# Performance work log

Measured on AMD Instinct MI355X. Metric: run time of the kernel, lower is better.

The kernel has to match this reference:

```python
import jax, jax.numpy as jnp
import numpy as np


def setup_inputs() -> dict:
    key = jax.random.key(0)
    ks = jax.random.split(key, 4)
    B, C, H, W = 8, 512, 128, 128
    K, D = 150, 512
    std = 0.02
    return {
        "x": jax.random.normal(ks[0], (B, C, H, W), dtype=jnp.float32),
        "cls_repr": jax.random.normal(ks[1], (1, K, D), dtype=jnp.float32) * std,
        "W_cls": jax.random.normal(ks[2], (D, D), dtype=jnp.float32) * std,
        "W_feat": jax.random.normal(ks[3], (D, D), dtype=jnp.float32) * std,
        "ln_gamma": jnp.ones((K,), dtype=jnp.float32),
        "ln_beta": jnp.zeros((K,), dtype=jnp.float32),
    }


def reference(x, cls_repr, W_cls, W_feat, ln_gamma, ln_beta):
    b, c, h, w = x.shape
    K = cls_repr.shape[1]
    # img_feat: [b, hw, c]
    img_feat = jnp.transpose(x, (0, 2, 3, 1)).reshape(b, h * w, c)
    cls = jnp.broadcast_to(cls_repr, (b, K, c))
    # coupled_attn: [b, K, hw]
    coupled_attn = jnp.einsum("bnc,bkc->bkn", img_feat, cls)
    # class-direction softmax over hw, feeds class offsets
    cls_attn = jax.nn.softmax(coupled_attn, axis=2)                 # [b,K,hw]
    cls_offset = jnp.einsum("bkn,bnc->bkc", cls_attn, img_feat) @ W_cls.T
    aligned_cls = cls + cls_offset                                   # [b,K,c]
    # position-direction softmax over K, feeds feature offsets
    pos_attn = jax.nn.softmax(coupled_attn, axis=1)                 # [b,K,hw]
    feat_offset = jnp.einsum("bkn,bkc->bnc", pos_attn, cls) @ W_feat.T
    aligned_feat = img_feat + feat_offset                            # [b,hw,c]
    # masks: [b, hw, K], LayerNorm over K
    masks = jnp.einsum("bnc,bkc->bnk", aligned_feat, aligned_cls)
    mu = jnp.mean(masks, axis=-1, keepdims=True)
    var = jnp.var(masks, axis=-1, keepdims=True)
    masks = (masks - mu) * jax.lax.rsqrt(var + 1e-5) * ln_gamma + ln_beta
    return jnp.transpose(masks, (0, 2, 1)).reshape(b, K, h, w)
```

## Files before the change

### kernel.cpp

```cpp
#include <hip/hip_runtime.h>
#include <math.h>

#define BB 8
#define CC 512
#define HWN 16384
#define KK 150
#define KP 160
#define NSEG 32
#define SEGN (HWN / NSEG)

typedef short bf8v __attribute__((ext_vector_type(8)));
typedef float f4v __attribute__((ext_vector_type(4)));

static __device__ inline unsigned short f2b(float f) {
  unsigned u = __float_as_uint(f);
  u += 0x7fffu + ((u >> 16) & 1u);
  return (unsigned short)(u >> 16);
}
static __device__ inline float b2f(unsigned short s) {
  return __uint_as_float(((unsigned)s) << 16);
}
static __device__ inline float b2fs(short s) { return b2f((unsigned short)s); }

__global__ __launch_bounds__(256) void t0_prep(const float* __restrict__ cls,
                                               unsigned short* __restrict__ cls16,
                                               unsigned short* __restrict__ MT16,
                                               unsigned short* __restrict__ AC16) {
  int i = blockIdx.x * 256 + threadIdx.x;
  if (i < KP * CC) {
    int k = i >> 9, c = i & 511;
    cls16[i] = (k < KK) ? f2b(cls[k * CC + c]) : 0;
  }
  if (i < BB * KP * KP) MT16[i] = 0;
  if (i < BB * (KP - KK) * CC) {
    int b = i / ((KP - KK) * CC);
    int r = i % ((KP - KK) * CC);
    int k = KK + (r >> 9);
    int c = r & 511;
    AC16[((size_t)b * KP + k) * CC + c] = 0;
  }
}

__global__ __launch_bounds__(256) void t1_transpose(const float* __restrict__ x,
                                                    unsigned short* __restrict__ xT) {
  __shared__ float ts[32][65];
  const int n0 = blockIdx.x * 64, c0 = blockIdx.y * 32, b = blockIdx.z;
  const int tid = threadIdx.x;
  const float* xb = x + (size_t)b * CC * HWN;
#pragma unroll
  for (int i = 0; i < 8; i++) {
    int e = tid + i * 256;
    int n = e & 63, c = e >> 6;
    ts[c][n] = xb[(size_t)(c0 + c) * HWN + n0 + n];
  }
  __syncthreads();
  unsigned short* xo = xT + (size_t)b * HWN * CC;
#pragma unroll
  for (int i = 0; i < 4; i++) {
    int e = tid + i * 256;
    int c2 = e & 15, n = e >> 4;
    unsigned vv = (unsigned)f2b(ts[2 * c2][n]) | ((unsigned)f2b(ts[2 * c2 + 1][n]) << 16);
    *(unsigned*)&xo[(size_t)(n0 + n) * CC + c0 + 2 * c2] = vv;
  }
}

__global__ __launch_bounds__(256) void g1_mfma(const unsigned short* __restrict__ xT,
                                               const unsigned short* __restrict__ cls16,
                                               unsigned short* __restrict__ A16,
                                               float* __restrict__ vvec) {
  const int n0 = blockIdx.x * 128, b = blockIdx.y;
  const int tid = threadIdx.x, w = tid >> 6, L = tid & 63;
  const int q = L >> 4, m16 = L & 15;
  f4v zf = {0.f, 0.f, 0.f, 0.f};
  f4v acc[10][2];
#pragma unroll
  for (int mt = 0; mt < 10; mt++) { acc[mt][0] = zf; acc[mt][1] = zf; }
  const unsigned short* xr0 = xT + ((size_t)(b * HWN + n0 + 32 * w + m16)) * CC + 8 * q;
  const unsigned short* xr1 = xr0 + 16 * CC;
  const unsigned short* cb = cls16 + (size_t)m16 * CC + 8 * q;
#pragma unroll 2
  for (int c0 = 0; c0 < CC; c0 += 32) {
    bf8v b0 = *(const bf8v*)(xr0 + c0);
    bf8v b1 = *(const bf8v*)(xr1 + c0);
#pragma unroll
    for (int mt = 0; mt < 10; mt++) {
      bf8v a = *(const bf8v*)(cb + (size_t)(16 * mt) * CC + c0);
      acc[mt][0] = __builtin_amdgcn_mfma_f32_16x16x32_bf16(a, b0, acc[mt][0], 0, 0, 0);
      acc[mt][1] = __builtin_amdgcn_mfma_f32_16x16x32_bf16(a, b1, acc[mt][1], 0, 0, 0);
    }
  }
#pragma unroll
  for (int mt = 0; mt < 10; mt++)
#pragma unroll
    for (int r = 0; r < 4; r++) {
      int k = 16 * mt + 4 * q + r;
      if (k < KK) {
        size_t row = ((size_t)(b * KK + k)) * HWN + n0 + 32 * w;
        A16[row + m16] = f2b(acc[mt][0][r]);
        A16[row + 16 + m16] = f2b(acc[mt][1][r]);
      }
    }
  float cm[2] = {-1e30f, -1e30f}, cs[2] = {0.f, 0.f};
  const int kq = 4 * q;
#pragma unroll
  for (int mt = 0; mt < 10; mt++)
#pragma unroll
    for (int r = 0; r < 4; r++) {
      bool valid = (16 * mt + kq + r) < KK;
#pragma unroll
      for (int nc = 0; nc < 2; nc++) {
        float a = valid ? acc[mt][nc][r] : -1e30f;
        cm[nc] = fmaxf(cm[nc], a);
      }
    }
#pragma unroll
  for (int mt = 0; mt < 10; mt++)
#pragma unroll
    for (int r = 0; r < 4; r++) {
      bool valid = (16 * mt + kq + r) < KK;
#pragma unroll
      for (int nc = 0; nc < 2; nc++)
        if (valid) cs[nc] += __expf(acc[mt][nc][r] - cm[nc]);
    }
#pragma unroll
  for (int off = 16; off < 64; off <<= 1) {
#pragma unroll
    for (int nc = 0; nc < 2; nc++) {
      float m2 = __shfl_xor(cm[nc], off, 64);
      float s2 = __shfl_xor(cs[nc], off, 64);
      float mn = fmaxf(cm[nc], m2);
      cs[nc] = cs[nc] * __expf(cm[nc] - mn) + s2 * __expf(m2 - mn);
      cm[nc] = mn;
    }
  }
  if (q == 0) {
#pragma unroll
    for (int nc = 0; nc < 2; nc++)
      vvec[b * HWN + n0 + 32 * w + 16 * nc + m16] = __expf(-cm[nc]) / cs[nc];
  }
}

__global__ __launch_bounds__(256) void g2a_rowstats(const unsigned short* __restrict__ A16,
                                                    float* __restrict__ rowmax,
                                                    float* __restrict__ rowsum) {
  const int bk = blockIdx.x;
  const bf8v* row = (const bf8v*)(A16 + (size_t)bk * HWN);
  __shared__ float red[8];
  const int tid = threadIdx.x, lane = tid & 63, w = tid >> 6;
  float m = -1e30f;
  for (int i = tid; i < HWN / 8; i += 256) {
    bf8v u = row[i];
#pragma unroll
    for (int j = 0; j < 8; j++) m = fmaxf(m, b2fs(u[j]));
  }
#pragma unroll
  for (int o = 32; o > 0; o >>= 1) m = fmaxf(m, __shfl_down(m, o, 64));
  if (lane == 0) red[w] = m;
  __syncthreads();
  if (tid == 0) red[4] = fmaxf(fmaxf(red[0], red[1]), fmaxf(red[2], red[3]));
  __syncthreads();
  const float mm = red[4];
  float s = 0.f;
  for (int i = tid; i < HWN / 8; i += 256) {
    bf8v u = row[i];
#pragma unroll
    for (int j = 0; j < 8; j++) s += __expf(b2fs(u[j]) - mm);
  }
#pragma unroll
  for (int o = 32; o > 0; o >>= 1) s += __shfl_down(s, o, 64);
  if (lane == 0) red[w] = s;
  __syncthreads();
  if (tid == 0) {
    rowmax[bk] = mm;
    rowsum[bk] = red[0] + red[1] + red[2] + red[3];
  }
}

__global__ __launch_bounds__(256) void e1_exp(const unsigned short* __restrict__ A16,
                                              const float* __restrict__ rowmax,
                                              unsigned short* __restrict__ E16,
                                              unsigned short* __restrict__ ET16) {
  const int n0 = blockIdx.x * 64, k0 = blockIdx.y * 32, b = blockIdx.z;
  const int tid = threadIdx.x;
  __shared__ unsigned short ls[64 * 33];
  const int kr = tid >> 3, n8 = tid & 7;
  const int k = k0 + kr;
  bf8v e;
  if (k < KK) {
    float rm = rowmax[b * KK + k];
    bf8v a = *(const bf8v*)&A16[((size_t)(b * KK + k)) * HWN + n0 + 8 * n8];
#pragma unroll
    for (int j = 0; j < 8; j++) e[j] = (short)f2b(__expf(b2fs(a[j]) - rm));
  } else {
#pragma unroll
    for (int j = 0; j < 8; j++) e[j] = 0;
  }
  *(bf8v*)&E16[((size_t)(b * KP + k)) * HWN + n0 + 8 * n8] = e;
#pragma unroll
  for (int j = 0; j < 8; j++) ls[(8 * n8 + j) * 33 + kr] = (unsigned short)e[j];
  __syncthreads();
  const int n = tid >> 2, k8 = tid & 3;
  bf8v o;
#pragma unroll
  for (int j = 0; j < 8; j++) o[j] = (short)ls[n * 33 + 8 * k8 + j];
  *(bf8v*)&ET16[((size_t)(b * HWN + n0 + n)) * KP + k0 + 8 * k8] = o;
}

__global__ __launch_bounds__(256) void g3_mfma(const float* __restrict__ x,
                                               const unsigned short* __restrict__ E16,
                                               float* __restrict__ Scp) {
  const int cblk = blockIdx.x, seg = blockIdx.y, b = blockIdx.z;
  const int tid = threadIdx.x, w = tid >> 6, L = tid & 63;
  const int q = L >> 4, m16 = L & 15;
  const int kgrp = w & 1, cgrp = w >> 1;
  f4v zf = {0.f, 0.f, 0.f, 0.f};
  f4v acc[5][4];
#pragma unroll
  for (int mt = 0; mt < 5; mt++)
#pragma unroll
    for (int cc = 0; cc < 4; cc++) acc[mt][cc] = zf;
  const unsigned short* eb = E16 + ((size_t)(b * KP + 80 * kgrp + m16)) * HWN + 8 * q;
  const float* xb = x + (size_t)b * CC * HWN +
                    (size_t)(cblk * 128 + 64 * cgrp + m16) * HWN + 8 * q;
  const int ns0 = seg * SEGN;
#pragma unroll 2
  for (int nc0 = ns0; nc0 < ns0 + SEGN; nc0 += 32) {
    bf8v af[5];
#pragma unroll
    for (int mt = 0; mt < 5; mt++)
      af[mt] = *(const bf8v*)(eb + (size_t)(16 * mt) * HWN + nc0);
#pragma unroll
    for (int cc = 0; cc < 4; cc++) {
      const float* xp = xb + (size_t)(16 * cc) * HWN + nc0;
      float4 x0 = *(const float4*)xp;
      float4 x1 = *(const float4*)(xp + 4);
      bf8v bf;
      bf[0] = (short)f2b(x0.x); bf[1] = (short)f2b(x0.y);
      bf[2] = (short)f2b(x0.z); bf[3] = (short)f2b(x0.w);
      bf[4] = (short)f2b(x1.x); bf[5] = (short)f2b(x1.y);
      bf[6] = (short)f2b(x1.z); bf[7] = (short)f2b(x1.w);
#pragma unroll
      for (int mt = 0; mt < 5; mt++)
        acc[mt][cc] = __builtin_amdgcn_mfma_f32_16x16x32_bf16(af[mt], bf, acc[mt][cc], 0, 0, 0);
    }
  }
#pragma unroll
  for (int mt = 0; mt < 5; mt++)
#pragma unroll
    for (int cc = 0; cc < 4; cc++)
#pragma unroll
      for (int r = 0; r < 4; r++) {
        int k = 80 * kgrp + 16 * mt + 4 * q + r;
        if (k < KK) {
          int c = cblk * 128 + 64 * cgrp + 16 * cc + m16;
          Scp[(((size_t)(b * NSEG + seg)) * KK + k) * CC + c] = acc[mt][cc][r];
        }
      }
}

__global__ __launch_bounds__(256) void g5_reduce(const float* __restrict__ Scp,
                                                 const float* __restrict__ rowsum,
                                                 float* __restrict__ Sc) {
  const int bk = blockIdx.x;
  const int b = bk / KK, k = bk % KK;
  const float inv = 1.0f / rowsum[bk];
  for (int c = threadIdx.x; c < CC; c += 256) {
    float s = 0.f;
    for (int g = 0; g < NSEG; g++)
      s += Scp[(((size_t)(b * NSEG + g)) * KK + k) * CC + c];
    Sc[(size_t)bk * CC + c] = s * inv;
  }
}

__global__ __launch_bounds__(256) void g4b_cwf(const float* __restrict__ cls,
                                               const float* __restrict__ Wf,
                                               float* __restrict__ CWf) {
  const int k = blockIdx.y;
  const int w = threadIdx.x >> 6, lane = threadIdx.x & 63;
  const int j0 = (blockIdx.x * 4 + w) * 4;
  const float4* arow = (const float4*)(cls + (size_t)k * CC);
  float4 a0 = arow[lane], a1 = arow[64 + lane];
#pragma unroll
  for (int jj = 0; jj < 4; jj++) {
    const float4* brow = (const float4*)(Wf + (size_t)(j0 + jj) * CC);
    float4 b0 = brow[lane], b1 = brow[64 + lane];
    float d = a0.x * b0.x + a0.y * b0.y + a0.z * b0.z + a0.w * b0.w +
              a1.x * b1.x + a1.y * b1.y + a1.z * b1.z + a1.w * b1.w;
#pragma unroll
    for (int o = 32; o > 0; o >>= 1) d += __shfl_down(d, o, 64);
    if (lane == 0) CWf[(size_t)k * CC + j0 + jj] = d;
  }
}

__global__ __launch_bounds__(256) void g4a_ac(const float* __restrict__ Sc,
                                              const float* __restrict__ Wc,
                                              const float* __restrict__ cls,
                                              float* __restrict__ AC,
                                              unsigned short* __restrict__ AC16) {
  const int bk = blockIdx.y;
  const int b = bk / KK, k = bk % KK;
  const int w = threadIdx.x >> 6, lane = threadIdx.x & 63;
  const int j0 = (blockIdx.x * 4 + w) * 4;
  const float4* arow = (const float4*)(Sc + (size_t)bk * CC);
  float4 a0 = arow[lane], a1 = arow[64 + lane];
#pragma unroll
  for (int jj = 0; jj < 4; jj++) {
    const float4* brow = (const float4*)(Wc + (size_t)(j0 + jj) * CC);
    float4 b0 = brow[lane], b1 = brow[64 + lane];
    float d = a0.x * b0.x + a0.y * b0.y + a0.z * b0.z + a0.w * b0.w +
              a1.x * b1.x + a1.y * b1.y + a1.z * b1.z + a1.w * b1.w;
#pragma unroll
    for (int o = 32; o > 0; o >>= 1) d += __shfl_down(d, o, 64);
    if (lane == 0) {
      float val = cls[k * CC + j0 + jj] + d;
      AC[(size_t)bk * CC + j0 + jj] = val;
      AC16[((size_t)b * KP + k) * CC + j0 + jj] = f2b(val);
    }
  }
}

__global__ __launch_bounds__(256) void g4c_m(const float* __restrict__ CWf,
                                             const float* __restrict__ AC,
                                             const float* __restrict__ rowmax,
                                             unsigned short* __restrict__ MT16) {
  const int k1 = blockIdx.y, b = blockIdx.z;
  const int w = threadIdx.x >> 6, lane = threadIdx.x & 63;
  const int k20 = (blockIdx.x * 4 + w) * 4;
  const float4* arow = (const float4*)(CWf + (size_t)k1 * CC);
  float4 a0 = arow[lane], a1 = arow[64 + lane];
  const float u = __expf(rowmax[b * KK + k1]);
#pragma unroll
  for (int jj = 0; jj < 4; jj++) {
    int k2 = k20 + jj;
    if (k2 >= KK) break;
    const float4* brow = (const float4*)(AC + (size_t)(b * KK + k2) * CC);
    float4 b0 = brow[lane], b1 = brow[64 + lane];
    float d = a0.x * b0.x + a0.y * b0.y + a0.z * b0.z + a0.w * b0.w +
              a1.x * b1.x + a1.y * b1.y + a1.z * b1.z + a1.w * b1.w;
#pragma unroll
    for (int o = 32; o > 0; o >>= 1) d += __shfl_down(d, o, 64);
    if (lane == 0) MT16[((size_t)b * KP + k2) * KP + k1] = f2b(d * u);
  }
}

__global__ __launch_bounds__(256) void g6_mfma(
    const unsigned short* __restrict__ xT, const unsigned short* __restrict__ ET,
    const float* __restrict__ vvec, const unsigned short* __restrict__ AC16,
    const unsigned short* __restrict__ MT16, const float* __restrict__ gamma,
    const float* __restrict__ beta, float* __restrict__ out) {
  const int n0 = blockIdx.x * 128, b = blockIdx.y;
  const int tid = threadIdx.x, w = tid >> 6, L = tid & 63;
  const int q = L >> 4, m16 = L & 15;
  f4v zf = {0.f, 0.f, 0.f, 0.f};
  f4v acc[10][2];
#pragma unroll
  for (int mt = 0; mt < 10; mt++) { acc[mt][0] = zf; acc[mt][1] = zf; }

  const unsigned short* et0 = ET + ((size_t)(b * HWN + n0 + 32 * w + m16)) * KP + 8 * q;
  const unsigned short* et1 = et0 + 16 * KP;
  const unsigned short* mb = MT16 + (size_t)b * KP * KP + (size_t)m16 * KP + 8 * q;
#pragma unroll
  for (int kc = 0; kc < KP; kc += 32) {
    bf8v b0 = *(const bf8v*)(et0 + kc);
    bf8v b1 = *(const bf8v*)(et1 + kc);
#pragma unroll
    for (int mt = 0; mt < 10; mt++) {
      bf8v a = *(const bf8v*)(mb + (size_t)(16 * mt) * KP + kc);
      acc[mt][0] = __builtin_amdgcn_mfma_f32_16x16x32_bf16(a, b0, acc[mt][0], 0, 0, 0);
      acc[mt][1] = __builtin_amdgcn_mfma_f32_16x16x32_bf16(a, b1, acc[mt][1], 0, 0, 0);
    }
  }
  const float v0 = vvec[b * HWN + n0 + 32 * w + m16];
  const float v1 = vvec[b * HWN + n0 + 32 * w + 16 + m16];
#pragma unroll
  for (int mt = 0; mt < 10; mt++)
#pragma unroll
    for (int r = 0; r < 4; r++) {
      acc[mt][0][r] *= v0;
      acc[mt][1][r] *= v1;
    }

  const unsigned short* xr0 = xT + ((size_t)(b * HWN + n0 + 32 * w + m16)) * CC + 8 * q;
  const unsigned short* xr1 = xr0 + 16 * CC;
  const unsigned short* ab = AC16 + (size_t)b * KP * CC + (size_t)m16 * CC + 8 * q;
#pragma unroll 2
  for (int c0 = 0; c0 < CC; c0 += 32) {
    bf8v b0 = *(const bf8v*)(xr0 + c0);
    bf8v b1 = *(const bf8v*)(xr1 + c0);
#pragma unroll
    for (int mt = 0; mt < 10; mt++) {
      bf8v a = *(const bf8v*)(ab + (size_t)(16 * mt) * CC + c0);
      acc[mt][0] = __builtin_amdgcn_mfma_f32_16x16x32_bf16(a, b0, acc[mt][0], 0, 0, 0);
      acc[mt][1] = __builtin_amdgcn_mfma_f32_16x16x32_bf16(a, b1, acc[mt][1], 0, 0, 0);
    }
  }

  float s1[2] = {0.f, 0.f}, s2[2] = {0.f, 0.f};
#pragma unroll
  for (int mt = 0; mt < 10; mt++)
#pragma unroll
    for (int r = 0; r < 4; r++)
#pragma unroll
      for (int nc = 0; nc < 2; nc++) {
        float a = acc[mt][nc][r];
        s1[nc] += a;
        s2[nc] += a * a;
      }
#pragma unroll
  for (int nc = 0; nc < 2; nc++) {
    s1[nc] += __shfl_xor(s1[nc], 16, 64);
    s1[nc] += __shfl_xor(s1[nc], 32, 64);
    s2[nc] += __shfl_xor(s2[nc], 16, 64);
    s2[nc] += __shfl_xor(s2[nc], 32, 64);
  }
  float mu[2], inv[2];
#pragma unroll
  for (int nc = 0; nc < 2; nc++) {
    mu[nc] = s1[nc] * (1.0f / KK);
    float var = s2[nc] * (1.0f / KK) - mu[nc] * mu[nc];
    inv[nc] = rsqrtf(var + 1e-5f);
  }
#pragma unroll
  for (int mt = 0; mt < 10; mt++)
#pragma unroll
    for (int r = 0; r < 4; r++) {
      int k = 16 * mt + 4 * q + r;
      if (k < KK) {
        float g = gamma[k], be = beta[k];
        size_t row = (size_t)(b * KK + k) * HWN + n0 + 32 * w;
        out[row + m16] = (acc[mt][0][r] - mu[0]) * inv[0] * g + be;
        out[row + 16 + m16] = (acc[mt][1][r] - mu[1]) * inv[1] * g + be;
      }
    }
}

extern "C" void kernel_launch(void* const* d_in, const int* in_sizes, int n_in,
                              void* d_out, int out_size, void* d_ws, size_t ws_size,
                              hipStream_t stream) {
  const float* x = (const float*)d_in[0];
  const float* cls = (const float*)d_in[1];
  const float* Wc = (const float*)d_in[2];
  const float* Wf = (const float*)d_in[3];
  const float* gam = (const float*)d_in[4];
  const float* bet = (const float*)d_in[5];
  float* out = (float*)d_out;

  char* p = (char*)d_ws;
  auto alloc = [&](size_t bytes) {
    char* r = p;
    p += (bytes + 255) & ~(size_t)255;
    return r;
  };
  unsigned short* xT16 = (unsigned short*)alloc((size_t)BB * HWN * CC * 2);
  unsigned short* A16 = (unsigned short*)alloc((size_t)BB * KK * HWN * 2);
  unsigned short* E16 = (unsigned short*)alloc((size_t)BB * KP * HWN * 2);
  unsigned short* ET16 = (unsigned short*)alloc((size_t)BB * HWN * KP * 2);
  float* Scp = (float*)alloc((size_t)BB * NSEG * KK * CC * 4);
  float* Sc = (float*)alloc((size_t)BB * KK * CC * 4);
  float* AC = (float*)alloc((size_t)BB * KK * CC * 4);
  unsigned short* AC16 = (unsigned short*)alloc((size_t)BB * KP * CC * 2);
  float* CWf = (float*)alloc((size_t)KK * CC * 4);
  unsigned short* cls16 = (unsigned short*)alloc((size_t)KP * CC * 2);
  unsigned short* MT16 = (unsigned short*)alloc((size_t)BB * KP * KP * 2);
  float* rowmax = (float*)alloc(BB * KK * 4);
  float* rowsum = (float*)alloc(BB * KK * 4);
  float* vvec = (float*)alloc((size_t)BB * HWN * 4);

  t0_prep<<<dim3((BB * KP * KP + 255) / 256), 256, 0, stream>>>(cls, cls16, MT16, AC16);
  t1_transpose<<<dim3(HWN / 64, CC / 32, BB), 256, 0, stream>>>(x, xT16);
  g1_mfma<<<dim3(HWN / 128, BB), 256, 0, stream>>>(xT16, cls16, A16, vvec);
  g2a_rowstats<<<dim3(BB * KK), 256, 0, stream>>>(A16, rowmax, rowsum);
  e1_exp<<<dim3(HWN / 64, KP / 32, BB), 256, 0, stream>>>(A16, rowmax, E16, ET16);
  g3_mfma<<<dim3(CC / 128, NSEG, BB), 256, 0, stream>>>(x, E16, Scp);
  g5_reduce<<<dim3(BB * KK), 256, 0, stream>>>(Scp, rowsum, Sc);
  g4b_cwf<<<dim3(CC / 16, KK), 256, 0, stream>>>(cls, Wf, CWf);
  g4a_ac<<<dim3(CC / 16, BB * KK), 256, 0, stream>>>(Sc, Wc, cls, AC, AC16);
  g4c_m<<<dim3(10, KK, BB), 256, 0, stream>>>(CWf, AC, rowmax, MT16);
  g6_mfma<<<dim3(HWN / 128, BB), 256, 0, stream>>>(xT16, ET16, vvec, AC16, MT16,
                                                   gam, bet, out);
}
```

Before: 930.8 us.

## Fuse softmax exp into first GEMM and move small matmuls to MFMA

The first GEMM now exponentiates its logits directly, with no max subtraction. It writes E16 and ET16, atomically accumulates row sums and computes the column inverse sums, so the A16 buffer and the rowstats and exp kernels are removed. The transpose kernel also writes a bf16 copy of x in the original layout, so g3 reads half the bytes and skips per-iteration conversion. The small class/weight projections (CWf, AC, MT) become bf16 MFMA GEMMs instead of per-dot-product wave reductions. Dropping the max subtraction risks overflow or precision loss if logits are large, and atomics add nondeterminism.

```diff
diff --git a/kernel.cpp b/kernel.cpp
--- a/kernel.cpp
+++ b/kernel.cpp
@@ -23,9 +23,14 @@
 static __device__ inline float b2fs(short s) { return b2f((unsigned short)s); }
 
 __global__ __launch_bounds__(256) void t0_prep(const float* __restrict__ cls,
+                                               const float* __restrict__ Wc,
+                                               const float* __restrict__ Wf,
                                                unsigned short* __restrict__ cls16,
+                                               unsigned short* __restrict__ Wc16,
+                                               unsigned short* __restrict__ Wf16,
                                                unsigned short* __restrict__ MT16,
-                                               unsigned short* __restrict__ AC16) {
+                                               unsigned short* __restrict__ AC16,
+                                               float* __restrict__ rowsum) {
   int i = blockIdx.x * 256 + threadIdx.x;
   if (i < KP * CC) {
     int k = i >> 9, c = i & 511;
@@ -39,19 +44,28 @@
     int c = r & 511;
     AC16[((size_t)b * KP + k) * CC + c] = 0;
   }
+  if (i < CC * CC) {
+    Wc16[i] = f2b(Wc[i]);
+    Wf16[i] = f2b(Wf[i]);
+  }
+  if (i < BB * KK) rowsum[i] = 0.f;
 }
 
 __global__ __launch_bounds__(256) void t1_transpose(const float* __restrict__ x,
-                                                    unsigned short* __restrict__ xT) {
+                                                    unsigned short* __restrict__ xT,
+                                                    unsigned short* __restrict__ x16) {
   __shared__ float ts[32][65];
   const int n0 = blockIdx.x * 64, c0 = blockIdx.y * 32, b = blockIdx.z;
   const int tid = threadIdx.x;
   const float* xb = x + (size_t)b * CC * HWN;
+  unsigned short* x16o = x16 + (size_t)b * CC * HWN;
 #pragma unroll
   for (int i = 0; i < 8; i++) {
     int e = tid + i * 256;
     int n = e & 63, c = e >> 6;
-    ts[c][n] = xb[(size_t)(c0 + c) * HWN + n0 + n];
+    float v = xb[(size_t)(c0 + c) * HWN + n0 + n];
+    ts[c][n] = v;
+    x16o[(size_t)(c0 + c) * HWN + n0 + n] = f2b(v);
   }
   __syncthreads();
   unsigned short* xo = xT + (size_t)b * HWN * CC;
@@ -66,8 +80,10 @@
 
 __global__ __launch_bounds__(256) void g1_mfma(const unsigned short* __restrict__ xT,
                                                const unsigned short* __restrict__ cls16,
-                                               unsigned short* __restrict__ A16,
-                                               float* __restrict__ vvec) {
+                                               unsigned short* __restrict__ E16,
+                                               unsigned short* __restrict__ ET16,
+                                               float* __restrict__ vvec,
+                                               float* __restrict__ rowsum) {
   const int n0 = blockIdx.x * 128, b = blockIdx.y;
   const int tid = threadIdx.x, w = tid >> 6, L = tid & 63;
   const int q = L >> 4, m16 = L & 15;
@@ -89,170 +105,84 @@
       acc[mt][1] = __builtin_amdgcn_mfma_f32_16x16x32_bf16(a, b1, acc[mt][1], 0, 0, 0);
     }
   }
-#pragma unroll
-  for (int mt = 0; mt < 10; mt++)
+  float cs0 = 0.f, cs1 = 0.f;
+  const int nA = n0 + 32 * w + m16;
+#pragma unroll
+  for (int mt = 0; mt < 10; mt++) {
+    unsigned short u0a[4], u1a[4];
 #pragma unroll
     for (int r = 0; r < 4; r++) {
       int k = 16 * mt + 4 * q + r;
-      if (k < KK) {
-        size_t row = ((size_t)(b * KK + k)) * HWN + n0 + 32 * w;
-        A16[row + m16] = f2b(acc[mt][0][r]);
-        A16[row + 16 + m16] = f2b(acc[mt][1][r]);
-      }
-    }
-  float cm[2] = {-1e30f, -1e30f}, cs[2] = {0.f, 0.f};
-  const int kq = 4 * q;
-#pragma unroll
-  for (int mt = 0; mt < 10; mt++)
-#pragma unroll
-    for (int r = 0; r < 4; r++) {
-      bool valid = (16 * mt + kq + r) < KK;
-#pragma unroll
-      for (int nc = 0; nc < 2; nc++) {
-        float a = valid ? acc[mt][nc][r] : -1e30f;
-        cm[nc] = fmaxf(cm[nc], a);
-      }
-    }
-#pragma unroll
-  for (int mt = 0; mt < 10; mt++)
-#pragma unroll
-    for (int r = 0; r < 4; r++) {
-      bool valid = (16 * mt + kq + r) < KK;
-#pragma unroll
-      for (int nc = 0; nc < 2; nc++)
-        if (valid) cs[nc] += __expf(acc[mt][nc][r] - cm[nc]);
-    }
-#pragma unroll
-  for (int off = 16; off < 64; off <<= 1) {
-#pragma unroll
-    for (int nc = 0; nc < 2; nc++) {
-      float m2 = __shfl_xor(cm[nc], off, 64);
-      float s2 = __shfl_xor(cs[nc], off, 64);
-      float mn = fmaxf(cm[nc], m2);
-      cs[nc] = cs[nc] * __expf(cm[nc] - mn) + s2 * __expf(m2 - mn);
-      cm[nc] = mn;
-    }
-  }
+      bool valid = k < KK;
+      float e0 = valid ? __expf(acc[mt][0][r]) : 0.f;
+      float e1 = valid ? __expf(acc[mt][1][r]) : 0.f;
+      cs0 += e0;
+      cs1 += e1;
+      unsigned short u0 = valid ? f2b(e0) : (unsigned short)0;
+      unsigned short u1 = valid ? f2b(e1) : (unsigned short)0;
+      u0a[r] = u0;
+      u1a[r] = u1;
+      size_t row = ((size_t)(b * KP + k)) * HWN + n0 + 32 * w;
+      E16[row + m16] = u0;
+      E16[row + 16 + m16] = u1;
+      float es = e0 + e1;
+      es += __shfl_xor(es, 1, 64);
+      es += __shfl_xor(es, 2, 64);
+      es += __shfl_xor(es, 4, 64);
+      es += __shfl_xor(es, 8, 64);
+      if (valid && m16 == 0) atomicAdd(&rowsum[b * KK + k], es);
+    }
+    unsigned lo0 = (unsigned)u0a[0] | ((unsigned)u0a[1] << 16);
+    unsigned hi0 = (unsigned)u0a[2] | ((unsigned)u0a[3] << 16);
+    unsigned lo1 = (unsigned)u1a[0] | ((unsigned)u1a[1] << 16);
+    unsigned hi1 = (unsigned)u1a[2] | ((unsigned)u1a[3] << 16);
+    size_t eoff = ((size_t)(b * HWN + nA)) * KP + 16 * mt + 4 * q;
+    *(uint2*)&ET16[eoff] = make_uint2(lo0, hi0);
+    *(uint2*)&ET16[eoff + (size_t)16 * KP] = make_uint2(lo1, hi1);
+  }
+  cs0 += __shfl_xor(cs0, 16, 64);
+  cs0 += __shfl_xor(cs0, 32, 64);
+  cs1 += __shfl_xor(cs1, 16, 64);
+  cs1 += __shfl_xor(cs1, 32, 64);
   if (q == 0) {
-#pragma unroll
-    for (int nc = 0; nc < 2; nc++)
-      vvec[b * HWN + n0 + 32 * w + 16 * nc + m16] = __expf(-cm[nc]) / cs[nc];
-  }
-}
-
-__global__ __launch_bounds__(256) void g2a_rowstats(const unsigned short* __restrict__ A16,
-                                                    float* __restrict__ rowmax,
-                                                    float* __restrict__ rowsum) {
-  const int bk = blockIdx.x;
-  const bf8v* row = (const bf8v*)(A16 + (size_t)bk * HWN);
-  __shared__ float red[8];
-  const int tid = threadIdx.x, lane = tid & 63, w = tid >> 6;
-  float m = -1e30f;
-  for (int i = tid; i < HWN / 8; i += 256) {
-    bf8v u = row[i];
-#pragma unroll
-    for (int j = 0; j < 8; j++) m = fmaxf(m, b2fs(u[j]));
-  }
-#pragma unroll
-  for (int o = 32; o > 0; o >>= 1) m = fmaxf(m, __shfl_down(m, o, 64));
-  if (lane == 0) red[w] = m;
-  __syncthreads();
-  if (tid == 0) red[4] = fmaxf(fmaxf(red[0], red[1]), fmaxf(red[2], red[3]));
-  __syncthreads();
-  const float mm = red[4];
-  float s = 0.f;
-  for (int i = tid; i < HWN / 8; i += 256) {
-    bf8v u = row[i];
-#pragma unroll
-    for (int j = 0; j < 8; j++) s += __expf(b2fs(u[j]) - mm);
-  }
-#pragma unroll
-  for (int o = 32; o > 0; o >>= 1) s += __shfl_down(s, o, 64);
-  if (lane == 0) red[w] = s;
-  __syncthreads();
-  if (tid == 0) {
-    rowmax[bk] = mm;
-    rowsum[bk] = red[0] + red[1] + red[2] + red[3];
-  }
-}
-
-__global__ __launch_bounds__(256) void e1_exp(const unsigned short* __restrict__ A16,
-                                              const float* __restrict__ rowmax,
-                                              unsigned short* __restrict__ E16,
-                                              unsigned short* __restrict__ ET16) {
-  const int n0 = blockIdx.x * 64, k0 = blockIdx.y * 32, b = blockIdx.z;
-  const int tid = threadIdx.x;
-  __shared__ unsigned short ls[64 * 33];
-  const int kr = tid >> 3, n8 = tid & 7;
-  const int k = k0 + kr;
-  bf8v e;
-  if (k < KK) {
-    float rm = rowmax[b * KK + k];
-    bf8v a = *(const bf8v*)&A16[((size_t)(b * KK + k)) * HWN + n0 + 8 * n8];
-#pragma unroll
-    for (int j = 0; j < 8; j++) e[j] = (short)f2b(__expf(b2fs(a[j]) - rm));
-  } else {
-#pragma unroll
-    for (int j = 0; j < 8; j++) e[j] = 0;
-  }
-  *(bf8v*)&E16[((size_t)(b * KP + k)) * HWN + n0 + 8 * n8] = e;
-#pragma unroll
-  for (int j = 0; j < 8; j++) ls[(8 * n8 + j) * 33 + kr] = (unsigned short)e[j];
-  __syncthreads();
-  const int n = tid >> 2, k8 = tid & 3;
-  bf8v o;
-#pragma unroll
-  for (int j = 0; j < 8; j++) o[j] = (short)ls[n * 33 + 8 * k8 + j];
-  *(bf8v*)&ET16[((size_t)(b * HWN + n0 + n)) * KP + k0 + 8 * k8] = o;
-}
-
-__global__ __launch_bounds__(256) void g3_mfma(const float* __restrict__ x,
+    vvec[b * HWN + nA] = 1.0f / cs0;
+    vvec[b * HWN + nA + 16] = 1.0f / cs1;
+  }
+}
+
+__global__ __launch_bounds__(256) void g3_mfma(const unsigned short* __restrict__ x16,
                                                const unsigned short* __restrict__ E16,
                                                float* __restrict__ Scp) {
   const int cblk = blockIdx.x, seg = blockIdx.y, b = blockIdx.z;
   const int tid = threadIdx.x, w = tid >> 6, L = tid & 63;
   const int q = L >> 4, m16 = L & 15;
-  const int kgrp = w & 1, cgrp = w >> 1;
-  f4v zf = {0.f, 0.f, 0.f, 0.f};
-  f4v acc[5][4];
-#pragma unroll
-  for (int mt = 0; mt < 5; mt++)
-#pragma unroll
-    for (int cc = 0; cc < 4; cc++) acc[mt][cc] = zf;
-  const unsigned short* eb = E16 + ((size_t)(b * KP + 80 * kgrp + m16)) * HWN + 8 * q;
-  const float* xb = x + (size_t)b * CC * HWN +
-                    (size_t)(cblk * 128 + 64 * cgrp + m16) * HWN + 8 * q;
+  f4v zf = {0.f, 0.f, 0.f, 0.f};
+  f4v acc[10][2];
+#pragma unroll
+  for (int mt = 0; mt < 10; mt++) { acc[mt][0] = zf; acc[mt][1] = zf; }
+  const unsigned short* eb = E16 + ((size_t)(b * KP + m16)) * HWN + 8 * q;
+  const unsigned short* xb = x16 + ((size_t)(b * CC + cblk * 128 + 32 * w + m16)) * HWN + 8 * q;
   const int ns0 = seg * SEGN;
 #pragma unroll 2
   for (int nc0 = ns0; nc0 < ns0 + SEGN; nc0 += 32) {
-    bf8v af[5];
-#pragma unroll
-    for (int mt = 0; mt < 5; mt++)
-      af[mt] = *(const bf8v*)(eb + (size_t)(16 * mt) * HWN + nc0);
-#pragma unroll
-    for (int cc = 0; cc < 4; cc++) {
-      const float* xp = xb + (size_t)(16 * cc) * HWN + nc0;
-      float4 x0 = *(const float4*)xp;
-      float4 x1 = *(const float4*)(xp + 4);
-      bf8v bf;
-      bf[0] = (short)f2b(x0.x); bf[1] = (short)f2b(x0.y);
-      bf[2] = (short)f2b(x0.z); bf[3] = (short)f2b(x0.w);
-      bf[4] = (short)f2b(x1.x); bf[5] = (short)f2b(x1.y);
-      bf[6] = (short)f2b(x1.z); bf[7] = (short)f2b(x1.w);
-#pragma unroll
-      for (int mt = 0; mt < 5; mt++)
-        acc[mt][cc] = __builtin_amdgcn_mfma_f32_16x16x32_bf16(af[mt], bf, acc[mt][cc], 0, 0, 0);
-    }
-  }
-#pragma unroll
-  for (int mt = 0; mt < 5; mt++)
-#pragma unroll
-    for (int cc = 0; cc < 4; cc++)
+    bf8v x0 = *(const bf8v*)(xb + nc0);
+    bf8v x1 = *(const bf8v*)(xb + (size_t)16 * HWN + nc0);
+#pragma unroll
+    for (int mt = 0; mt < 10; mt++) {
+      bf8v a = *(const bf8v*)(eb + (size_t)(16 * mt) * HWN + nc0);
+      acc[mt][0] = __builtin_amdgcn_mfma_f32_16x16x32_bf16(a, x0, acc[mt][0], 0, 0, 0);
+      acc[mt][1] = __builtin_amdgcn_mfma_f32_16x16x32_bf16(a, x1, acc[mt][1], 0, 0, 0);
+    }
+  }
+#pragma unroll
+  for (int mt = 0; mt < 10; mt++)
+#pragma unroll
+    for (int cc = 0; cc < 2; cc++)
 #pragma unroll
       for (int r = 0; r < 4; r++) {
-        int k = 80 * kgrp + 16 * mt + 4 * q + r;
+        int k = 16 * mt + 4 * q + r;
         if (k < KK) {
-          int c = cblk * 128 + 64 * cgrp + 16 * cc + m16;
+          int c = cblk * 128 + 32 * w + 16 * cc + m16;
           Scp[(((size_t)(b * NSEG + seg)) * KK + k) * CC + c] = acc[mt][cc][r];
         }
       }
@@ -260,7 +190,7 @@
 
 __global__ __launch_bounds__(256) void g5_reduce(const float* __restrict__ Scp,
                                                  const float* __restrict__ rowsum,
-                                                 float* __restrict__ Sc) {
+                                                 unsigned short* __restrict__ Sc16) {
   const int bk = blockIdx.x;
   const int b = bk / KK, k = bk % KK;
   const float inv = 1.0f / rowsum[bk];
@@ -268,79 +198,114 @@
     float s = 0.f;
     for (int g = 0; g < NSEG; g++)
       s += Scp[(((size_t)(b * NSEG + g)) * KK + k) * CC + c];
-    Sc[(size_t)bk * CC + c] = s * inv;
-  }
-}
-
-__global__ __launch_bounds__(256) void g4b_cwf(const float* __restrict__ cls,
-                                               const float* __restrict__ Wf,
-                                               float* __restrict__ CWf) {
-  const int k = blockIdx.y;
-  const int w = threadIdx.x >> 6, lane = threadIdx.x & 63;
-  const int j0 = (blockIdx.x * 4 + w) * 4;
-  const float4* arow = (const float4*)(cls + (size_t)k * CC);
-  float4 a0 = arow[lane], a1 = arow[64 + lane];
-#pragma unroll
-  for (int jj = 0; jj < 4; jj++) {
-    const float4* brow = (const float4*)(Wf + (size_t)(j0 + jj) * CC);
-    float4 b0 = brow[lane], b1 = brow[64 + lane];
-    float d = a0.x * b0.x + a0.y * b0.y + a0.z * b0.z + a0.w * b0.w +
-              a1.x * b1.x + a1.y * b1.y + a1.z * b1.z + a1.w * b1.w;
-#pragma unroll
-    for (int o = 32; o > 0; o >>= 1) d += __shfl_down(d, o, 64);
-    if (lane == 0) CWf[(size_t)k * CC + j0 + jj] = d;
-  }
-}
-
-__global__ __launch_bounds__(256) void g4a_ac(const float* __restrict__ Sc,
-                                              const float* __restrict__ Wc,
+    Sc16[((size_t)b * KP + k) * CC + c] = f2b(s * inv);
+  }
+}
+
+__global__ __launch_bounds__(256) void g4b_cwf(const unsigned short* __restrict__ cls16,
+                                               const unsigned short* __restrict__ Wf16,
+                                               unsigned short* __restrict__ CWf16) {
+  const int tid = threadIdx.x, w = tid >> 6, L = tid & 63;
+  const int q = L >> 4, m16 = L & 15;
+  const int j0 = blockIdx.x * 128 + 32 * w;
+  f4v zf = {0.f, 0.f, 0.f, 0.f};
+  f4v acc[10][2];
+#pragma unroll
+  for (int mt = 0; mt < 10; mt++) { acc[mt][0] = zf; acc[mt][1] = zf; }
+  const unsigned short* ar = cls16 + (size_t)m16 * CC + 8 * q;
+  const unsigned short* br = Wf16 + (size_t)(j0 + m16) * CC + 8 * q;
+#pragma unroll 2
+  for (int c0 = 0; c0 < CC; c0 += 32) {
+    bf8v b0 = *(const bf8v*)(br + c0);
+    bf8v b1 = *(const bf8v*)(br + (size_t)16 * CC + c0);
+#pragma unroll
+    for (int mt = 0; mt < 10; mt++) {
+      bf8v a = *(const bf8v*)(ar + (size_t)(16 * mt) * CC + c0);
+      acc[mt][0] = __builtin_amdgcn_mfma_f32_16x16x32_bf16(a, b0, acc[mt][0], 0, 0, 0);
+      acc[mt][1] = __builtin_amdgcn_mfma_f32_16x16x32_bf16(a, b1, acc[mt][1], 0, 0, 0);
+    }
+  }
+#pragma unroll
+  for (int mt = 0; mt < 10; mt++)
+#pragma unroll
+    for (int nc = 0; nc < 2; nc++)
+#pragma unroll
+      for (int r = 0; r < 4; r++) {
+        int k1 = 16 * mt + 4 * q + r;
+        int j = j0 + 16 * nc + m16;
+        CWf16[(size_t)k1 * CC + j] = f2b(acc[mt][nc][r]);
+      }
+}
+
+__global__ __launch_bounds__(256) void g4a_ac(const unsigned short* __restrict__ Sc16,
+                                              const unsigned short* __restrict__ Wc16,
                                               const float* __restrict__ cls,
-                                              float* __restrict__ AC,
                                               unsigned short* __restrict__ AC16) {
-  const int bk = blockIdx.y;
-  const int b = bk / KK, k = bk % KK;
-  const int w = threadIdx.x >> 6, lane = threadIdx.x & 63;
-  const int j0 = (blockIdx.x * 4 + w) * 4;
-  const float4* arow = (const float4*)(Sc + (size_t)bk * CC);
-  float4 a0 = arow[lane], a1 = arow[64 + lane];
-#pragma unroll
-  for (int jj = 0; jj < 4; jj++) {
-    const float4* brow = (const float4*)(Wc + (size_t)(j0 + jj) * CC);
-    float4 b0 = brow[lane], b1 = brow[64 + lane];
-    float d = a0.x * b0.x + a0.y * b0.y + a0.z * b0.z + a0.w * b0.w +
-              a1.x * b1.x + a1.y * b1.y + a1.z * b1.z + a1.w * b1.w;
-#pragma unroll
-    for (int o = 32; o > 0; o >>= 1) d += __shfl_down(d, o, 64);
-    if (lane == 0) {
-      float val = cls[k * CC + j0 + jj] + d;
-      AC[(size_t)bk * CC + j0 + jj] = val;
-      AC16[((size_t)b * KP + k) * CC + j0 + jj] = f2b(val);
-    }
-  }
-}
-
-__global__ __launch_bounds__(256) void g4c_m(const float* __restrict__ CWf,
-                                             const float* __restrict__ AC,
-                                             const float* __restrict__ rowmax,
+  const int b = blockIdx.y;
+  const int tid = threadIdx.x, w = tid >> 6, L = tid & 63;
+  const int q = L >> 4, m16 = L & 15;
+  const int j0 = blockIdx.x * 128 + 32 * w;
+  f4v zf = {0.f, 0.f, 0.f, 0.f};
+  f4v acc[10][2];
+#pragma unroll
+  for (int mt = 0; mt < 10; mt++) { acc[mt][0] = zf; acc[mt][1] = zf; }
+  const unsigned short* ar = Sc16 + ((size_t)b * KP + m16) * CC + 8 * q;
+  const unsigned short* br = Wc16 + (size_t)(j0 + m16) * CC + 8 * q;
+#pragma unroll 2
+  for (int c0 = 0; c0 < CC; c0 += 32) {
+    bf8v b0 = *(const bf8v*)(br + c0);
+    bf8v b1 = *(const bf8v*)(br + (size_t)16 * CC + c0);
+#pragma unroll
+    for (int mt = 0; mt < 10; mt++) {
+      bf8v a = *(const bf8v*)(ar + (size_t)(16 * mt) * CC + c0);
+      acc[mt][0] = __builtin_amdgcn_mfma_f32_16x16x32_bf16(a, b0, acc[mt][0], 0, 0, 0);
+      acc[mt][1] = __builtin_amdgcn_mfma_f32_16x16x32_bf16(a, b1, acc[mt][1], 0, 0, 0);
+    }
+  }
+#pragma unroll
+  for (int mt = 0; mt < 10; mt++)
+#pragma unroll
+    for (int nc = 0; nc < 2; nc++)
+#pragma unroll
+      for (int r = 0; r < 4; r++) {
+        int k = 16 * mt + 4 * q + r;
+        if (k < KK) {
+          int j = j0 + 16 * nc + m16;
+          AC16[((size_t)b * KP + k) * CC + j] = f2b(cls[k * CC + j] + acc[mt][nc][r]);
+        }
+      }
+}
+
+__global__ __launch_bounds__(256) void g4c_m(const unsigned short* __restrict__ AC16,
+                                             const unsigned short* __restrict__ CWf16,
                                              unsigned short* __restrict__ MT16) {
-  const int k1 = blockIdx.y, b = blockIdx.z;
-  const int w = threadIdx.x >> 6, lane = threadIdx.x & 63;
-  const int k20 = (blockIdx.x * 4 + w) * 4;
-  const float4* arow = (const float4*)(CWf + (size_t)k1 * CC);
-  float4 a0 = arow[lane], a1 = arow[64 + lane];
-  const float u = __expf(rowmax[b * KK + k1]);
-#pragma unroll
-  for (int jj = 0; jj < 4; jj++) {
-    int k2 = k20 + jj;
-    if (k2 >= KK) break;
-    const float4* brow = (const float4*)(AC + (size_t)(b * KK + k2) * CC);
-    float4 b0 = brow[lane], b1 = brow[64 + lane];
-    float d = a0.x * b0.x + a0.y * b0.y + a0.z * b0.z + a0.w * b0.w +
-              a1.x * b1.x + a1.y * b1.y + a1.z * b1.z + a1.w * b1.w;
-#pragma unroll
-    for (int o = 32; o > 0; o >>= 1) d += __shfl_down(d, o, 64);
-    if (lane == 0) MT16[((size_t)b * KP + k2) * KP + k1] = f2b(d * u);
-  }
+  const int b = blockIdx.y;
+  const int tid = threadIdx.x, w = tid >> 6, L = tid & 63;
+  const int q = L >> 4, m16 = L & 15;
+  const int k1t = blockIdx.x * 64 + 16 * w;
+  f4v zf = {0.f, 0.f, 0.f, 0.f};
+  f4v acc[10];
+#pragma unroll
+  for (int mt = 0; mt < 10; mt++) acc[mt] = zf;
+  const unsigned short* ar = AC16 + ((size_t)b * KP + m16) * CC + 8 * q;
+  const unsigned short* br = CWf16 + (size_t)(k1t + m16) * CC + 8 * q;
+#pragma unroll 2
+  for (int c0 = 0; c0 < CC; c0 += 32) {
+    bf8v bb = *(const bf8v*)(br + c0);
+#pragma unroll
+    for (int mt = 0; mt < 10; mt++) {
+      bf8v a = *(const bf8v*)(ar + (size_t)(16 * mt) * CC + c0);
+      acc[mt] = __builtin_amdgcn_mfma_f32_16x16x32_bf16(a, bb, acc[mt], 0, 0, 0);
+    }
+  }
+  const int k1 = k1t + m16;
+#pragma unroll
+  for (int mt = 0; mt < 10; mt++)
+#pragma unroll
+    for (int r = 0; r < 4; r++) {
+      int k2 = 16 * mt + 4 * q + r;
+      if (k1 < KK) MT16[((size_t)b * KP + k2) * KP + k1] = f2b(acc[mt][r]);
+    }
 }
 
 __global__ __launch_bounds__(256) void g6_mfma(
@@ -452,30 +417,29 @@
     return r;
   };
   unsigned short* xT16 = (unsigned short*)alloc((size_t)BB * HWN * CC * 2);
-  unsigned short* A16 = (unsigned short*)alloc((size_t)BB * KK * HWN * 2);
+  unsigned short* x16 = (unsigned short*)alloc((size_t)BB * CC * HWN * 2);
   unsigned short* E16 = (unsigned short*)alloc((size_t)BB * KP * HWN * 2);
   unsigned short* ET16 = (unsigned short*)alloc((size_t)BB * HWN * KP * 2);
   float* Scp = (float*)alloc((size_t)BB * NSEG * KK * CC * 4);
-  float* Sc = (float*)alloc((size_t)BB * KK * CC * 4);
-  float* AC = (float*)alloc((size_t)BB * KK * CC * 4);
+  unsigned short* Sc16 = (unsigned short*)alloc((size_t)BB * KP * CC * 2);
   unsigned short* AC16 = (unsigned short*)alloc((size_t)BB * KP * CC * 2);
-  float* CWf = (float*)alloc((size_t)KK * CC * 4);
+  unsigned short* CWf16 = (unsigned short*)alloc((size_t)192 * CC * 2);
   unsigned short* cls16 = (unsigned short*)alloc((size_t)KP * CC * 2);
+  unsigned short* Wc16 = (unsigned short*)alloc((size_t)CC * CC * 2);
+  unsigned short* Wf16 = (unsigned short*)alloc((size_t)CC * CC * 2);
   unsigned short* MT16 = (unsigned short*)alloc((size_t)BB * KP * KP * 2);
-  float* rowmax = (float*)alloc(BB * KK * 4);
   float* rowsum = (float*)alloc(BB * KK * 4);
   float* vvec = (float*)alloc((size_t)BB * HWN * 4);
 
-  t0_prep<<<dim3((BB * KP * KP + 255) / 256), 256, 0, stream>>>(cls, cls16, MT16, AC16);
-  t1_transpose<<<dim3(HWN / 64, CC / 32, BB), 256, 0, stream>>>(x, xT16);
-  g1_mfma<<<dim3(HWN / 128, BB), 256, 0, stream>>>(xT16, cls16, A16, vvec);
-  g2a_rowstats<<<dim3(BB * KK), 256, 0, stream>>>(A16, rowmax, rowsum);
-  e1_exp<<<dim3(HWN / 64, KP / 32, BB), 256, 0, stream>>>(A16, rowmax, E16, ET16);
-  g3_mfma<<<dim3(CC / 128, NSEG, BB), 256, 0, stream>>>(x, E16, Scp);
-  g5_reduce<<<dim3(BB * KK), 256, 0, stream>>>(Scp, rowsum, Sc);
-  g4b_cwf<<<dim3(CC / 16, KK), 256, 0, stream>>>(cls, Wf, CWf);
-  g4a_ac<<<dim3(CC / 16, BB * KK), 256, 0, stream>>>(Sc, Wc, cls, AC, AC16);
-  g4c_m<<<dim3(10, KK, BB), 256, 0, stream>>>(CWf, AC, rowmax, MT16);
+  t0_prep<<<dim3((CC * CC + 255) / 256), 256, 0, stream>>>(cls, Wc, Wf, cls16, Wc16,
+                                                           Wf16, MT16, AC16, rowsum);
+  t1_transpose<<<dim3(HWN / 64, CC / 32, BB), 256, 0, stream>>>(x, xT16, x16);
+  g1_mfma<<<dim3(HWN / 128, BB), 256, 0, stream>>>(xT16, cls16, E16, ET16, vvec, rowsum);
+  g4b_cwf<<<dim3(CC / 128), 256, 0, stream>>>(cls16, Wf16, CWf16);
+  g3_mfma<<<dim3(CC / 128, NSEG, BB), 256, 0, stream>>>(x16, E16, Scp);
+  g5_reduce<<<dim3(BB * KK), 256, 0, stream>>>(Scp, rowsum, Sc16);
+  g4a_ac<<<dim3(CC / 128, BB), 256, 0, stream>>>(Sc16, Wc16, cls, AC16);
+  g4c_m<<<dim3(3, BB), 256, 0, stream>>>(AC16, CWf16, MT16);
   g6_mfma<<<dim3(HWN / 128, BB), 256, 0, stream>>>(xT16, ET16, vvec, AC16, MT16,
                                                    gam, bet, out);
 }
```

New measurement: 1.101 ms. 1.18x slower.
